# Kernel tuning notes

Hardware: AMD Instinct MI355X
Metric: run time of the kernel (lower is better)

The kernel has to match this reference:

```python
import jax, jax.numpy as jnp
import numpy as np

EMBED = 768
HEADS = 12
FACTOR = 2
LN_EPS = 1e-5


def layer_norm(x, gamma, beta):
    mu = jnp.mean(x, axis=-1, keepdims=True)
    var = jnp.mean(jnp.square(x - mu), axis=-1, keepdims=True)
    return (x - mu) * jax.lax.rsqrt(var + LN_EPS) * gamma + beta


def setup_inputs() -> dict:
    key = jax.random.key(0)
    ks = jax.random.split(key, 8)
    B, S, E = 8, 1024, EMBED
    H = FACTOR * E
    s_e = 1.0 / np.sqrt(E)
    s_h = 1.0 / np.sqrt(H)
    return {
        "x": jax.random.normal(ks[0], (B, S, E), jnp.float32),
        "Wq": jax.random.normal(ks[1], (E, E), jnp.float32) * s_e,
        "Wk": jax.random.normal(ks[2], (E, E), jnp.float32) * s_e,
        "Wv": jax.random.normal(ks[3], (E, E), jnp.float32) * s_e,
        "W1": jax.random.normal(ks[4], (E, H), jnp.float32) * s_e,
        "b1": jnp.zeros((H,), jnp.float32),
        "W2": jax.random.normal(ks[5], (H, E), jnp.float32) * s_h,
        "b2": jnp.zeros((E,), jnp.float32),
        "g1": jnp.ones((E,), jnp.float32),
        "beta1": jnp.zeros((E,), jnp.float32),
        "g2": jnp.ones((E,), jnp.float32),
        "beta2": jnp.zeros((E,), jnp.float32),
    }


def reference(x, Wq, Wk, Wv, W1, b1, W2, b2, g1, beta1, g2, beta2):
    B, S, E = x.shape
    hd = E // HEADS
    # NOTE: original reshapes (B,S,E)->(B,H,S,hd) WITHOUT transposing heads
    # (non-standard: mixes sequence blocks across heads) - replicated faithfully.
    q = (x @ Wq).reshape(B, HEADS, S, hd)
    k = (x @ Wk).reshape(B, HEADS, S, hd)
    v = (x @ Wv).reshape(B, HEADS, S, hd)
    # no 1/sqrt(d) scaling in the original
    attn = jax.nn.softmax(jnp.einsum('bnqd,bnkd->bnqk', q, k), axis=-1)
    # NOTE: original einsum 'bnqk,bnvd->bnqd' sums over BOTH k and v
    # (value is sum-pooled over its sequence axis) - replicated faithfully.
    out = jnp.einsum('bnqk,bnvd->bnqd', attn, v)
    out = out.transpose(0, 2, 1, 3).reshape(B, S, E)
    a = x + layer_norm(out, g1, beta1)
    # GELU after BOTH linears (exact GELU, torch default)
    h = jax.nn.gelu(a @ W1 + b1, approximate=False)
    m = jax.nn.gelu(h @ W2 + b2, approximate=False)
    return x + layer_norm(m, g2, beta2)
```

## Files before the change

kernel.cpp:

```cpp
#include <hip/hip_runtime.h>
#include <hip/hip_bf16.h>
#include <math.h>

#define E_ 768
#define HID_ 1536
#define SQ_ 1024

typedef unsigned short u16;
using bf16x8 = __attribute__((ext_vector_type(8))) __bf16;
using f32x4  = __attribute__((ext_vector_type(4))) float;

__device__ __forceinline__ u16 f2bf(float f) {
  union { float f; unsigned u; } v; v.f = f;
  unsigned r = v.u + 0x7FFFu + ((v.u >> 16) & 1u);
  return (u16)(r >> 16);
}
__device__ __forceinline__ float bf2f(u16 h) {
  union { unsigned u; float f; } v; v.u = ((unsigned)h) << 16; return v.f;
}
__device__ __forceinline__ float gelu_f(float x) {
  return 0.5f * x * (1.0f + erff(x * 0.70710678118654752f));
}

#define GLDS16(gp, sp) __builtin_amdgcn_global_load_lds( \
    (__attribute__((address_space(1))) const void*)(const void*)(gp), \
    (__attribute__((address_space(3))) void*)(void*)(sp), 16, 0, 0)

__global__ void prep_kernel(const float* __restrict__ x, const float* __restrict__ W1,
                            const float* __restrict__ W2, u16* __restrict__ xb,
                            u16* __restrict__ W1T, u16* __restrict__ W2T) {
  __shared__ float T[64 * 65];
  int bid = blockIdx.x, t = threadIdx.x;
  if (bid < 6144) {
    int base = bid * 1024 + t * 4;
    const float4 v = *reinterpret_cast<const float4*>(x + base);
    ushort4 o; o.x = f2bf(v.x); o.y = f2bf(v.y); o.z = f2bf(v.z); o.w = f2bf(v.w);
    *reinterpret_cast<ushort4*>(xb + base) = o;
    return;
  }
  const float* in; u16* out; int R_in, C_in, rt, ct;
  if (bid < 6432) {
    int b2 = bid - 6144; in = W1; out = W1T; R_in = 768; C_in = 1536;
    rt = b2 / 24; ct = b2 % 24;
  } else {
    int b3 = bid - 6432; in = W2; out = W2T; R_in = 1536; C_in = 768;
    rt = b3 / 12; ct = b3 % 12;
  }
  int r0 = rt << 6, c0 = ct << 6;
  int tr = t >> 4, tc4 = (t & 15) << 2;
#pragma unroll
  for (int i = 0; i < 4; ++i) {
    int row = tr + (i << 4);
    const float4 v = *reinterpret_cast<const float4*>(in + (size_t)(r0 + row) * C_in + c0 + tc4);
    T[row * 65 + tc4 + 0] = v.x;
    T[row * 65 + tc4 + 1] = v.y;
    T[row * 65 + tc4 + 2] = v.z;
    T[row * 65 + tc4 + 3] = v.w;
  }
  __syncthreads();
#pragma unroll
  for (int i = 0; i < 4; ++i) {
    int orow = tr + (i << 4);
    ushort4 o;
    o.x = f2bf(T[(tc4 + 0) * 65 + orow]);
    o.y = f2bf(T[(tc4 + 1) * 65 + orow]);
    o.z = f2bf(T[(tc4 + 2) * 65 + orow]);
    o.w = f2bf(T[(tc4 + 3) * 65 + orow]);
    *reinterpret_cast<ushort4*>(out + (size_t)(c0 + orow) * R_in + r0 + tc4) = o;
  }
}

__global__ void rowsum_kernel(const u16* __restrict__ xb, float* __restrict__ Rp) {
  int bid = blockIdx.x;
  int r = bid >> 2, c = bid & 3;
  int b = r / 12, n = r % 12;
  int t = threadIdx.x;
  int u0 = n << 10;
  int s_lo = u0 / 12;
  int s_hi = (u0 + 1023) / 12;
  int cnt = s_hi - s_lo + 1;
  int cs = s_lo + (cnt * c) / 4;
  int ce = s_lo + (cnt * (c + 1)) / 4;
  float acc[12][3];
#pragma unroll
  for (int g = 0; g < 12; ++g)
    for (int q = 0; q < 3; ++q) acc[g][q] = 0.f;
  const u16* xp = xb + (size_t)b * SQ_ * E_;
  for (int s = cs; s < ce; ++s) {
    float v0 = bf2f(xp[(size_t)s * E_ + t]);
    float v1 = bf2f(xp[(size_t)s * E_ + t + 256]);
    float v2 = bf2f(xp[(size_t)s * E_ + t + 512]);
    int du = 12 * s - u0;
#pragma unroll
    for (int g = 0; g < 12; ++g) {
      int u = du + g;
      if (u >= 0 && u < 1024) { acc[g][0] += v0; acc[g][1] += v1; acc[g][2] += v2; }
    }
  }
  float* Rr = Rp + (size_t)bid * 9216;
#pragma unroll
  for (int g = 0; g < 12; ++g) {
    Rr[g * 768 + t]       = acc[g][0];
    Rr[g * 768 + t + 256] = acc[g][1];
    Rr[g * 768 + t + 512] = acc[g][2];
  }
}

__global__ void ygemm_kernel(const float* __restrict__ Rp, const float* __restrict__ Wv,
                             float* __restrict__ P3) {
  int g = blockIdx.x, r = blockIdx.y, jc = blockIdx.z;
  int t = threadIdx.x;
  int d = t & 63, sub = t >> 6;
  const float* R0 = Rp + (size_t)r * 4 * 9216 + g * 768;
  const float* wp = Wv + g * 64 + d;
  int j0 = jc * 96 + sub * 24;
  float a0 = 0.f, a1 = 0.f, a2 = 0.f, a3 = 0.f;
#pragma unroll
  for (int jj = 0; jj < 24; jj += 4) {
    int j = j0 + jj;
    float r0v = R0[j + 0] + R0[9216 + j + 0] + R0[18432 + j + 0] + R0[27648 + j + 0];
    float r1v = R0[j + 1] + R0[9216 + j + 1] + R0[18432 + j + 1] + R0[27648 + j + 1];
    float r2v = R0[j + 2] + R0[9216 + j + 2] + R0[18432 + j + 2] + R0[27648 + j + 2];
    float r3v = R0[j + 3] + R0[9216 + j + 3] + R0[18432 + j + 3] + R0[27648 + j + 3];
    a0 += r0v * wp[(size_t)(j + 0) * 768];
    a1 += r1v * wp[(size_t)(j + 1) * 768];
    a2 += r2v * wp[(size_t)(j + 2) * 768];
    a3 += r3v * wp[(size_t)(j + 3) * 768];
  }
  __shared__ float red[256];
  red[t] = (a0 + a1) + (a2 + a3);
  __syncthreads();
  if (sub == 0)
    P3[(((size_t)r * 12 + g) * 8 + jc) * 64 + d] = red[d] + red[64 + d] + red[128 + d] + red[192 + d];
}

__global__ void ysum_kernel(const float* __restrict__ P3, float* __restrict__ Y) {
  int bn = blockIdx.x;
  int t = threadIdx.x;
  int d = t & 63, sub = t >> 6;
  const float* Pp = P3 + (size_t)bn * 6144 + d;
  int g0 = sub * 24;
  float s = 0.f;
#pragma unroll 8
  for (int gj = 0; gj < 24; ++gj) s += Pp[(g0 + gj) << 6];
  __shared__ float red[256];
  red[t] = s;
  __syncthreads();
  if (sub == 0)
    Y[bn * 64 + d] = red[d] + red[64 + d] + red[128 + d] + red[192 + d];
}

__global__ void c1_kernel(const float* __restrict__ Y, const float* __restrict__ g1,
                          const float* __restrict__ be1, const float* __restrict__ W1,
                          const float* __restrict__ b1, float* __restrict__ C1) {
  int bid = blockIdx.x;
  int b = bid / 48, c = bid % 48;
  int t = threadIdx.x;
  __shared__ float Ls[768];
  __shared__ float red[8][32];
  __shared__ float red2[8];
  float y0 = Y[b * 768 + t];
  float y1 = Y[b * 768 + t + 256];
  float y2 = Y[b * 768 + t + 512];
  float s = y0 + y1 + y2;
  float sq = y0 * y0 + y1 * y1 + y2 * y2;
#pragma unroll
  for (int o = 32; o > 0; o >>= 1) { s += __shfl_down(s, o, 64); sq += __shfl_down(sq, o, 64); }
  if ((t & 63) == 0) { red2[(t >> 6) * 2] = s; red2[(t >> 6) * 2 + 1] = sq; }
  __syncthreads();
  s  = red2[0] + red2[2] + red2[4] + red2[6];
  sq = red2[1] + red2[3] + red2[5] + red2[7];
  float mu = s * (1.f / 768.f);
  float var = sq * (1.f / 768.f) - mu * mu;
  float rsv = rsqrtf(var + 1e-5f);
  Ls[t]       = (y0 - mu) * rsv * g1[t]       + be1[t];
  Ls[t + 256] = (y1 - mu) * rsv * g1[t + 256] + be1[t + 256];
  Ls[t + 512] = (y2 - mu) * rsv * g1[t + 512] + be1[t + 512];
  __syncthreads();
  int tc = t & 31, ts = t >> 5;
  int n = c * 32 + tc;
  float acc = 0.f;
  int j0 = ts * 96;
#pragma unroll 4
  for (int j = j0; j < j0 + 96; ++j) acc += Ls[j] * W1[(size_t)j * HID_ + n];
  red[ts][tc] = acc;
  __syncthreads();
  if (ts == 0) {
    float sv = b1[n];
#pragma unroll
    for (int k = 0; k < 8; ++k) sv += red[k][tc];
    C1[b * HID_ + n] = sv;
  }
}

template <int MODE>
__global__ __launch_bounds__(256, 2) void gemm_bt_kernel(
    const u16* __restrict__ A, const u16* __restrict__ BT,
    const float* __restrict__ bias, void* __restrict__ out0, void* __restrict__ out1,
    int N, int lda, int ldb) {
  __shared__ __align__(16) u16 As[2][128 * 64];
  __shared__ __align__(16) u16 Bs[2][128 * 64];
  int bid = blockIdx.x;
  int xcd = bid & 7, idx = bid >> 3;
  int mloc, n_, k_off, kk = 0;
  if (MODE == 0) { mloc = idx / 12; n_ = idx % 12; k_off = 0; }
  else           { kk = idx / 48; int rem = idx % 48; mloc = rem / 6; n_ = rem % 6; k_off = kk * 768; }
  int bm = (xcd * 8 + mloc) << 7, bn = n_ << 7;

  int t = threadIdx.x;
  int lane = t & 63, w = t >> 6;
  int wm = (w >> 1) << 6, wn = (w & 1) << 6;
  int quad = lane >> 4, l16 = lane & 15;
  f32x4 acc[4][4] = {};

  const u16* Ab = A + (size_t)bm * lda + k_off;
  const u16* Bb = BT + (size_t)bn * ldb + k_off;

  auto STAGE = [&](int buf, int k0) {
#pragma unroll
    for (int i = 0; i < 4; ++i) {
      int ci = t + (i << 8);
      int r = ci >> 3, csw = ci & 7;
      int kc = csw ^ (r & 7);
      GLDS16(Ab + (size_t)r * lda + k0 + (kc << 3), &As[buf][ci << 3]);
      GLDS16(Bb + (size_t)r * ldb + k0 + (kc << 3), &Bs[buf][ci << 3]);
    }
  };

  STAGE(0, 0);
  __syncthreads();

#pragma unroll 2
  for (int tt = 0; tt < 12; ++tt) {
    int buf = tt & 1;
    if (tt < 11) STAGE(buf ^ 1, (tt + 1) << 6);
    const u16* as = As[buf];
    const u16* bs = Bs[buf];
#pragma unroll
    for (int ks = 0; ks < 2; ++ks) {
      bf16x8 af[4], bf[4];
      int kc = (ks << 2) + quad;
#pragma unroll
      for (int mt = 0; mt < 4; ++mt) {
        int row = wm + (mt << 4) + l16;
        af[mt] = *reinterpret_cast<const bf16x8*>(as + row * 64 + ((kc ^ (row & 7)) << 3));
      }
#pragma unroll
      for (int nt = 0; nt < 4; ++nt) {
        int row = wn + (nt << 4) + l16;
        bf[nt] = *reinterpret_cast<const bf16x8*>(bs + row * 64 + ((kc ^ (row & 7)) << 3));
      }
#pragma unroll
      for (int mt = 0; mt < 4; ++mt)
#pragma unroll
        for (int nt = 0; nt < 4; ++nt)
          acc[mt][nt] = __builtin_amdgcn_mfma_f32_16x16x32_bf16(af[mt], bf[nt], acc[mt][nt], 0, 0, 0);
    }
    __syncthreads();
  }

#pragma unroll
  for (int mt = 0; mt < 4; ++mt) {
    int row0 = bm + wm + (mt << 4) + (quad << 2);
#pragma unroll
    for (int nt = 0; nt < 4; ++nt) {
      int col = bn + wn + (nt << 4) + l16;
      float bv = (MODE == 0) ? bias[(bm >> 10) * N + col] : 0.f;
#pragma unroll
      for (int rr = 0; rr < 4; ++rr) {
        float v = acc[mt][nt][rr] + bv;
        size_t idxo = (size_t)(row0 + rr) * N + col;
        if (MODE == 0)       ((u16*)out0)[idxo] = f2bf(gelu_f(v));
        else if (kk == 0)    ((u16*)out0)[idxo] = f2bf(v);
        else                 ((u16*)out1)[idxo] = f2bf(v);
      }
    }
  }
}

__global__ void ln2_kernel(const u16* __restrict__ p0, const u16* __restrict__ p1,
                           const float* __restrict__ x, const float* __restrict__ b2,
                           const float* __restrict__ g2, const float* __restrict__ be2,
                           float* __restrict__ out) {
  int row = blockIdx.x, t = threadIdx.x;
  float v0 = 0.f, v1 = 0.f, v2 = 0.f, v3 = 0.f;
  float s = 0.f, sq = 0.f;
  int e = t << 2;
  if (t < 192) {
    ushort4 pa = *reinterpret_cast<const ushort4*>(p0 + (size_t)row * 768 + e);
    ushort4 pb = *reinterpret_cast<const ushort4*>(p1 + (size_t)row * 768 + e);
    float4 bb = *reinterpret_cast<const float4*>(b2 + e);
    v0 = gelu_f(bf2f(pa.x) + bf2f(pb.x) + bb.x);
    v1 = gelu_f(bf2f(pa.y) + bf2f(pb.y) + bb.y);
    v2 = gelu_f(bf2f(pa.z) + bf2f(pb.z) + bb.z);
    v3 = gelu_f(bf2f(pa.w) + bf2f(pb.w) + bb.w);
    s = (v0 + v1) + (v2 + v3);
    sq = (v0 * v0 + v1 * v1) + (v2 * v2 + v3 * v3);
  }
  __shared__ float red[8];
#pragma unroll
  for (int o = 32; o > 0; o >>= 1) { s += __shfl_down(s, o, 64); sq += __shfl_down(sq, o, 64); }
  if ((t & 63) == 0) { red[(t >> 6) * 2] = s; red[(t >> 6) * 2 + 1] = sq; }
  __syncthreads();
  s  = red[0] + red[2] + red[4];
  sq = red[1] + red[3] + red[5];
  float mu = s * (1.f / 768.f);
  float var = sq * (1.f / 768.f) - mu * mu;
  float rs = rsqrtf(var + 1e-5f);
  if (t < 192) {
    float4 gg = *reinterpret_cast<const float4*>(g2 + e);
    float4 be = *reinterpret_cast<const float4*>(be2 + e);
    float4 xx = *reinterpret_cast<const float4*>(x + (size_t)row * 768 + e);
    float4 o;
    o.x = xx.x + (v0 - mu) * rs * gg.x + be.x;
    o.y = xx.y + (v1 - mu) * rs * gg.y + be.y;
    o.z = xx.z + (v2 - mu) * rs * gg.z + be.z;
    o.w = xx.w + (v3 - mu) * rs * gg.w + be.w;
    *reinterpret_cast<float4*>(out + (size_t)row * 768 + e) = o;
  }
}

extern "C" void kernel_launch(void* const* d_in, const int* in_sizes, int n_in,
                              void* d_out, int out_size, void* d_ws, size_t ws_size,
                              hipStream_t stream) {
  const float* x   = (const float*)d_in[0];
  const float* Wv  = (const float*)d_in[3];
  const float* W1  = (const float*)d_in[4];
  const float* b1  = (const float*)d_in[5];
  const float* W2  = (const float*)d_in[6];
  const float* b2  = (const float*)d_in[7];
  const float* g1  = (const float*)d_in[8];
  const float* be1 = (const float*)d_in[9];
  const float* g2  = (const float*)d_in[10];
  const float* be2 = (const float*)d_in[11];
  float* out = (float*)d_out;

  char* ws = (char*)d_ws;
  u16*   xb  = (u16*)(ws);
  u16*   W1T = (u16*)(ws + 12582912);
  u16*   W2T = (u16*)(ws + 14942208);
  u16*   h   = (u16*)(ws + 17301504);
  float* Rp  = (float*)(ws + 17301504);
  float* P3  = (float*)(ws + 42467328);
  float* Y   = (float*)(ws + 44826624);
  float* C1  = (float*)(ws + 44875776);
  u16*   m0  = (u16*)(ws + 44924928);
  u16*   p1  = xb;

  prep_kernel<<<6720, 256, 0, stream>>>(x, W1, W2, xb, W1T, W2T);
  rowsum_kernel<<<384, 256, 0, stream>>>(xb, Rp);
  ygemm_kernel<<<dim3(12, 96, 8), 256, 0, stream>>>(Rp, Wv, P3);
  ysum_kernel<<<96, 256, 0, stream>>>(P3, Y);
  c1_kernel<<<384, 256, 0, stream>>>(Y, g1, be1, W1, b1, C1);
  gemm_bt_kernel<0><<<768, 256, 0, stream>>>(xb, W1T, C1, (void*)h, nullptr, 1536, 768, 768);
  gemm_bt_kernel<1><<<768, 256, 0, stream>>>(h, W2T, nullptr, (void*)m0, (void*)p1, 768, 1536, 1536);
  ln2_kernel<<<8192, 256, 0, stream>>>(m0, p1, x, b2, g2, be2, out);
}
```

Before: 251.1 us.

## Fuse value-path kernels into one and drop GEMM double buffering

Merges the rowsum, ygemm and ysum kernels into a single ypath kernel that keeps the row sums in shared memory and reduces directly to Y. This removes two launches and the large Rp/P3 intermediate round trips through global memory, but it runs only 96 blocks, each doing a long serial loop. Separately, the bf16 GEMM drops its double-buffered LDS staging for a single buffer with an explicit wait and barriers. That halves LDS use but exposes global-load latency with no overlap against the MFMA work.

```diff
diff --git a/kernel.cpp b/kernel.cpp
--- a/kernel.cpp
+++ b/kernel.cpp
@@ -70,84 +70,67 @@
   }
 }
 
-__global__ void rowsum_kernel(const u16* __restrict__ xb, float* __restrict__ Rp) {
-  int bid = blockIdx.x;
-  int r = bid >> 2, c = bid & 3;
+__global__ void ypath_kernel(const u16* __restrict__ xb, const float* __restrict__ Wv,
+                             float* __restrict__ Y) {
+  int r = blockIdx.x;
   int b = r / 12, n = r % 12;
   int t = threadIdx.x;
   int u0 = n << 10;
   int s_lo = u0 / 12;
   int s_hi = (u0 + 1023) / 12;
-  int cnt = s_hi - s_lo + 1;
-  int cs = s_lo + (cnt * c) / 4;
-  int ce = s_lo + (cnt * (c + 1)) / 4;
   float acc[12][3];
 #pragma unroll
   for (int g = 0; g < 12; ++g)
     for (int q = 0; q < 3; ++q) acc[g][q] = 0.f;
   const u16* xp = xb + (size_t)b * SQ_ * E_;
-  for (int s = cs; s < ce; ++s) {
+  for (int s = s_lo; s <= s_hi; ++s) {
     float v0 = bf2f(xp[(size_t)s * E_ + t]);
     float v1 = bf2f(xp[(size_t)s * E_ + t + 256]);
     float v2 = bf2f(xp[(size_t)s * E_ + t + 512]);
     int du = 12 * s - u0;
-#pragma unroll
-    for (int g = 0; g < 12; ++g) {
-      int u = du + g;
-      if (u >= 0 && u < 1024) { acc[g][0] += v0; acc[g][1] += v1; acc[g][2] += v2; }
+    if (du >= 0 && du <= 1012) {
+#pragma unroll
+      for (int g = 0; g < 12; ++g) { acc[g][0] += v0; acc[g][1] += v1; acc[g][2] += v2; }
+    } else {
+#pragma unroll
+      for (int g = 0; g < 12; ++g) {
+        int u = du + g;
+        if (u >= 0 && u < 1024) { acc[g][0] += v0; acc[g][1] += v1; acc[g][2] += v2; }
+      }
     }
   }
-  float* Rr = Rp + (size_t)bid * 9216;
+  __shared__ float Ls[12 * 768];
 #pragma unroll
   for (int g = 0; g < 12; ++g) {
-    Rr[g * 768 + t]       = acc[g][0];
-    Rr[g * 768 + t + 256] = acc[g][1];
-    Rr[g * 768 + t + 512] = acc[g][2];
-  }
-}
-
-__global__ void ygemm_kernel(const float* __restrict__ Rp, const float* __restrict__ Wv,
-                             float* __restrict__ P3) {
-  int g = blockIdx.x, r = blockIdx.y, jc = blockIdx.z;
-  int t = threadIdx.x;
+    Ls[g * 768 + t]       = acc[g][0];
+    Ls[g * 768 + t + 256] = acc[g][1];
+    Ls[g * 768 + t + 512] = acc[g][2];
+  }
+  __syncthreads();
   int d = t & 63, sub = t >> 6;
-  const float* R0 = Rp + (size_t)r * 4 * 9216 + g * 768;
-  const float* wp = Wv + g * 64 + d;
-  int j0 = jc * 96 + sub * 24;
-  float a0 = 0.f, a1 = 0.f, a2 = 0.f, a3 = 0.f;
-#pragma unroll
-  for (int jj = 0; jj < 24; jj += 4) {
+  float part[12];
+#pragma unroll
+  for (int g = 0; g < 12; ++g) part[g] = 0.f;
+  int j0 = sub * 192;
+  for (int jj = 0; jj < 192; ++jj) {
     int j = j0 + jj;
-    float r0v = R0[j + 0] + R0[9216 + j + 0] + R0[18432 + j + 0] + R0[27648 + j + 0];
-    float r1v = R0[j + 1] + R0[9216 + j + 1] + R0[18432 + j + 1] + R0[27648 + j + 1];
-    float r2v = R0[j + 2] + R0[9216 + j + 2] + R0[18432 + j + 2] + R0[27648 + j + 2];
-    float r3v = R0[j + 3] + R0[9216 + j + 3] + R0[18432 + j + 3] + R0[27648 + j + 3];
-    a0 += r0v * wp[(size_t)(j + 0) * 768];
-    a1 += r1v * wp[(size_t)(j + 1) * 768];
-    a2 += r2v * wp[(size_t)(j + 2) * 768];
-    a3 += r3v * wp[(size_t)(j + 3) * 768];
-  }
-  __shared__ float red[256];
-  red[t] = (a0 + a1) + (a2 + a3);
-  __syncthreads();
-  if (sub == 0)
-    P3[(((size_t)r * 12 + g) * 8 + jc) * 64 + d] = red[d] + red[64 + d] + red[128 + d] + red[192 + d];
-}
-
-__global__ void ysum_kernel(const float* __restrict__ P3, float* __restrict__ Y) {
-  int bn = blockIdx.x;
-  int t = threadIdx.x;
-  int d = t & 63, sub = t >> 6;
-  const float* Pp = P3 + (size_t)bn * 6144 + d;
-  int g0 = sub * 24;
-  float s = 0.f;
-#pragma unroll 8
-  for (int gj = 0; gj < 24; ++gj) s += Pp[(g0 + gj) << 6];
-  __shared__ float red[256];
-  red[t] = s;
-  __syncthreads();
-  if (sub == 0)
-    Y[bn * 64 + d] = red[d] + red[64 + d] + red[128 + d] + red[192 + d];
+    const float* wp = Wv + (size_t)j * 768 + d;
+#pragma unroll
+    for (int g = 0; g < 12; ++g)
+      part[g] += Ls[g * 768 + j] * wp[g * 64];
+  }
+  __shared__ float red[4][12][64];
+#pragma unroll
+  for (int g = 0; g < 12; ++g) red[sub][g][d] = part[g];
+  __syncthreads();
+  if (t < 64) {
+    float s = 0.f;
+#pragma unroll
+    for (int su = 0; su < 4; ++su)
+#pragma unroll
+      for (int g = 0; g < 12; ++g) s += red[su][g][t];
+    Y[r * 64 + t] = s;
+  }
 }
 
 __global__ void c1_kernel(const float* __restrict__ Y, const float* __restrict__ g1,
@@ -198,8 +181,8 @@
     const u16* __restrict__ A, const u16* __restrict__ BT,
     const float* __restrict__ bias, void* __restrict__ out0, void* __restrict__ out1,
     int N, int lda, int ldb) {
-  __shared__ __align__(16) u16 As[2][128 * 64];
-  __shared__ __align__(16) u16 Bs[2][128 * 64];
+  __shared__ __align__(16) u16 As[128 * 64];
+  __shared__ __align__(16) u16 Bs[128 * 64];
   int bid = blockIdx.x;
   int xcd = bid & 7, idx = bid >> 3;
   int mloc, n_, k_off, kk = 0;
@@ -213,29 +196,20 @@
   int quad = lane >> 4, l16 = lane & 15;
   f32x4 acc[4][4] = {};
 
-  const u16* Ab = A + (size_t)bm * lda + k_off;
-  const u16* Bb = BT + (size_t)bn * ldb + k_off;
-
-  auto STAGE = [&](int buf, int k0) {
+  for (int k0 = 0; k0 < 768; k0 += 64) {
+    __syncthreads();
 #pragma unroll
     for (int i = 0; i < 4; ++i) {
       int ci = t + (i << 8);
       int r = ci >> 3, csw = ci & 7;
       int kc = csw ^ (r & 7);
-      GLDS16(Ab + (size_t)r * lda + k0 + (kc << 3), &As[buf][ci << 3]);
-      GLDS16(Bb + (size_t)r * ldb + k0 + (kc << 3), &Bs[buf][ci << 3]);
+      const u16* ga = A + (size_t)(bm + r) * lda + k_off + k0 + (kc << 3);
+      GLDS16(ga, As + ci * 8);
+      const u16* gb = BT + (size_t)(bn + r) * ldb + k_off + k0 + (kc << 3);
+      GLDS16(gb, Bs + ci * 8);
     }
-  };
-
-  STAGE(0, 0);
-  __syncthreads();
-
-#pragma unroll 2
-  for (int tt = 0; tt < 12; ++tt) {
-    int buf = tt & 1;
-    if (tt < 11) STAGE(buf ^ 1, (tt + 1) << 6);
-    const u16* as = As[buf];
-    const u16* bs = Bs[buf];
+    __builtin_amdgcn_s_waitcnt(0);
+    __syncthreads();
 #pragma unroll
     for (int ks = 0; ks < 2; ++ks) {
       bf16x8 af[4], bf[4];
@@ -243,12 +217,12 @@
 #pragma unroll
       for (int mt = 0; mt < 4; ++mt) {
         int row = wm + (mt << 4) + l16;
-        af[mt] = *reinterpret_cast<const bf16x8*>(as + row * 64 + ((kc ^ (row & 7)) << 3));
+        af[mt] = *reinterpret_cast<const bf16x8*>(As + row * 64 + ((kc ^ (row & 7)) << 3));
       }
 #pragma unroll
       for (int nt = 0; nt < 4; ++nt) {
         int row = wn + (nt << 4) + l16;
-        bf[nt] = *reinterpret_cast<const bf16x8*>(bs + row * 64 + ((kc ^ (row & 7)) << 3));
+        bf[nt] = *reinterpret_cast<const bf16x8*>(Bs + row * 64 + ((kc ^ (row & 7)) << 3));
       }
 #pragma unroll
       for (int mt = 0; mt < 4; ++mt)
@@ -256,7 +230,6 @@
         for (int nt = 0; nt < 4; ++nt)
           acc[mt][nt] = __builtin_amdgcn_mfma_f32_16x16x32_bf16(af[mt], bf[nt], acc[mt][nt], 0, 0, 0);
     }
-    __syncthreads();
   }
 
 #pragma unroll
@@ -340,17 +313,13 @@
   u16*   W1T = (u16*)(ws + 12582912);
   u16*   W2T = (u16*)(ws + 14942208);
   u16*   h   = (u16*)(ws + 17301504);
-  float* Rp  = (float*)(ws + 17301504);
-  float* P3  = (float*)(ws + 42467328);
-  float* Y   = (float*)(ws + 44826624);
-  float* C1  = (float*)(ws + 44875776);
-  u16*   m0  = (u16*)(ws + 44924928);
+  float* Y   = (float*)(ws + 42467328);
+  float* C1  = (float*)(ws + 42491904);
+  u16*   m0  = (u16*)(ws + 42541056);
   u16*   p1  = xb;
 
   prep_kernel<<<6720, 256, 0, stream>>>(x, W1, W2, xb, W1T, W2T);
-  rowsum_kernel<<<384, 256, 0, stream>>>(xb, Rp);
-  ygemm_kernel<<<dim3(12, 96, 8), 256, 0, stream>>>(Rp, Wv, P3);
-  ysum_kernel<<<96, 256, 0, stream>>>(P3, Y);
+  ypath_kernel<<<96, 256, 0, stream>>>(xb, Wv, Y);
   c1_kernel<<<384, 256, 0, stream>>>(Y, g1, be1, W1, b1, C1);
   gemm_bt_kernel<0><<<768, 256, 0, stream>>>(xb, W1T, C1, (void*)h, nullptr, 1536, 768, 768);
   gemm_bt_kernel<1><<<768, 256, 0, stream>>>(h, W2T, nullptr, (void*)m0, (void*)p1, 768, 1536, 1536);
```

New measurement: 249.0 us. Within noise of the previous version (-0.8%).
